# Kernel tuning notes

Measured on AMD Instinct MI355X. Metric: run time of the kernel, lower is better.

The kernel has to match this reference:

```python
import jax, jax.numpy as jnp
import numpy as np

B, T, D_IN, E, H = 2, 2048, 1024, 64, 16  # batch, num_tokens, input dim, emb_size(per-head), num_heads


def setup_inputs() -> dict:
    key = jax.random.key(0)
    ks = jax.random.split(key, 6)
    s = 0.02
    inp = jax.random.normal(ks[0], (B, T, D_IN), dtype=jnp.float32)
    # causal mask: 1.0 where attention is disallowed (j > i), matching `scaled_compat -= mask * 1e9`
    mask = jnp.triu(jnp.ones((T, T), dtype=jnp.float32), k=1)
    Wq = jax.random.normal(ks[1], (D_IN, E * H), dtype=jnp.float32) * s
    Wk = jax.random.normal(ks[2], (D_IN, E * H), dtype=jnp.float32) * s
    Wv = jax.random.normal(ks[3], (D_IN, E * H), dtype=jnp.float32) * s
    Wu = jax.random.normal(ks[4], (E * H, E), dtype=jnp.float32) * s
    bu = jnp.zeros((E,), dtype=jnp.float32)
    return {"inp": inp, "mask": mask, "Wq": Wq, "Wk": Wk, "Wv": Wv, "Wu": Wu, "bu": bu}


def reference(inp, mask, Wq, Wk, Wv, Wu, bu):
    b = inp.shape[0]
    q = inp @ Wq  # [B,T,E*H]
    k = inp @ Wk
    v = inp @ Wv
    # NOTE: original reshapes last dim as (E, H) -> heads on fastest axis (interleaved layout)
    q = q.reshape(b, T, E, H)
    k = k.reshape(b, T, E, H)
    v = v.reshape(b, T, E, H)
    scores = jnp.einsum("bteh,bseh->bhts", q, k) / jnp.sqrt(jnp.float32(E))  # [B,H,T,T]
    if mask is not None:
        scores = scores - mask * 1e9
    attn = jax.nn.softmax(scores, axis=-1)
    wv = jnp.einsum("bhts,bseh->bhte", attn, v)  # [B,H,T,E]
    # transpose [0,2,3,1] -> [B,T,E,H], then flatten to [B,T,E*H] (H fastest, matching original)
    wv = jnp.transpose(wv, (0, 2, 3, 1)).reshape(b, T, E * H)
    return wv @ Wu + bu  # unify Dense(emb_size), with bias
```

## Files before the change

kernel.cpp:

```cpp
#include <hip/hip_runtime.h>


typedef __bf16 bf16x8 __attribute__((ext_vector_type(8)));
typedef float f32x4 __attribute__((ext_vector_type(4)));
typedef unsigned short u16;
typedef unsigned int u32;

#define AS1 __attribute__((address_space(1)))
#define AS3 __attribute__((address_space(3)))

__device__ __forceinline__ void gll16(const void* g, void* l) {
    __builtin_amdgcn_global_load_lds((const AS1 u32*)g, (AS3 u32*)l, 16, 0, 0);
}

__device__ __forceinline__ u16 f2bf(float f) {
    union { float f; u32 u; } v; v.f = f;
    u32 r = (v.u + 0x7FFFu + ((v.u >> 16) & 1u)) >> 16;
    return (u16)r;
}

#define MM 4096
#define SCALE_LOG2E 0.18033688011112042f

__global__ void cast_x(const float* __restrict__ in, u16* __restrict__ out, int n4) {
    int i = blockIdx.x * blockDim.x + threadIdx.x;
    if (i < n4) {
        float4 f = ((const float4*)in)[i];
        ushort4 o;
        o.x = f2bf(f.x); o.y = f2bf(f.y); o.z = f2bf(f.z); o.w = f2bf(f.w);
        ((ushort4*)out)[i] = o;
    }
}

__global__ void transpose_w(const float* __restrict__ Wq, const float* __restrict__ Wk,
                            const float* __restrict__ Wv, const float* __restrict__ Wu,
                            u16* __restrict__ wqt, u16* __restrict__ wkt,
                            u16* __restrict__ wvt, u16* __restrict__ wut) {
    int z = blockIdx.z;
    const float* src; u16* dst; int N;
    if (z == 0)      { src = Wq; dst = wqt; N = 1024; }
    else if (z == 1) { src = Wk; dst = wkt; N = 1024; }
    else if (z == 2) { src = Wv; dst = wvt; N = 1024; }
    else             { src = Wu; dst = wut; N = 64; if (blockIdx.y >= 2) return; }
    __shared__ float lds[32][33];
    int k0 = blockIdx.x * 32, n0 = blockIdx.y * 32;
    int tid = threadIdx.x;
    int c = tid & 31, r0 = tid >> 5;
#pragma unroll
    for (int p = 0; p < 4; ++p) {
        int r = r0 + p * 8;
        lds[r][c] = src[(k0 + r) * N + n0 + c];
    }
    __syncthreads();
#pragma unroll
    for (int p = 0; p < 4; ++p) {
        int n = n0 + r0 + p * 8;
        if (z < 3) {
            int rnew = ((n & 15) << 6) | (n >> 4);
            dst[rnew * 1024 + k0 + c] = f2bf(lds[c][n - n0]);
        } else {
            int k = k0 + c;
            int kp = ((k & 15) << 6) | (k >> 4);
            dst[n * 1024 + kp] = f2bf(lds[c][n - n0]);
        }
    }
}

__global__ __launch_bounds__(256) void gemm_qkv(const u16* __restrict__ xb,
                                                const u16* __restrict__ wqt,
                                                const u16* __restrict__ wkt,
                                                const u16* __restrict__ wvt,
                                                u16* __restrict__ qh, u16* __restrict__ kh,
                                                u16* __restrict__ vh) {
    int z = blockIdx.z;
    const u16* wt = (z == 0) ? wqt : (z == 1) ? wkt : wvt;
    u16* dst      = (z == 0) ? qh  : (z == 1) ? kh  : vh;
    __shared__ u16 lA[3][128 * 32];
    __shared__ u16 lB[3][128 * 32];
    int tid = threadIdx.x;
    int m0 = blockIdx.x * 128, n0 = blockIdx.y * 128;
    int lane = tid & 63, w = tid >> 6;
    int wr = w >> 1, wc = w & 1;
    int l15 = lane & 15, quad = lane >> 4;
    f32x4 acc[4][4] = {};
    int srow = tid >> 2, scol = (tid & 3) * 8;
    const u16* ga = xb + (m0 + srow) * 1024 + scol;
    const u16* gb = wt + (n0 + srow) * 1024 + scol;
#pragma unroll
    for (int t0 = 0; t0 < 2; ++t0)
#pragma unroll
        for (int pp = 0; pp < 2; ++pp) {
            gll16(ga + pp * 65536 + t0 * 32, lA[t0] + (pp * 256 + tid) * 8);
            gll16(gb + pp * 65536 + t0 * 32, lB[t0] + (pp * 256 + tid) * 8);
        }
    int cur = 0;
#pragma unroll 1
    for (int kk = 0; kk < 32; ++kk) {
        if (kk < 31) asm volatile("s_waitcnt vmcnt(4)" ::: "memory");
        else         asm volatile("s_waitcnt vmcnt(0)" ::: "memory");
        __builtin_amdgcn_s_barrier();
        if (kk + 2 < 32) {
            int nxt = cur + 2; if (nxt >= 3) nxt -= 3;
            int kb = (kk + 2) * 32;
#pragma unroll
            for (int pp = 0; pp < 2; ++pp) {
                gll16(ga + pp * 65536 + kb, lA[nxt] + (pp * 256 + tid) * 8);
                gll16(gb + pp * 65536 + kb, lB[nxt] + (pp * 256 + tid) * 8);
            }
        }
        bf16x8 af[4], bfr[4];
#pragma unroll
        for (int i = 0; i < 4; ++i)
            af[i] = *(const bf16x8*)(lA[cur] + (wr * 64 + i * 16 + l15) * 32 + quad * 8);
#pragma unroll
        for (int j = 0; j < 4; ++j)
            bfr[j] = *(const bf16x8*)(lB[cur] + (wc * 64 + j * 16 + l15) * 32 + quad * 8);
#pragma unroll
        for (int i = 0; i < 4; ++i)
#pragma unroll
            for (int j = 0; j < 4; ++j)
                acc[i][j] = __builtin_amdgcn_mfma_f32_16x16x32_bf16(af[i], bfr[j], acc[i][j], 0, 0, 0);
        ++cur; if (cur == 3) cur = 0;
    }
    int bb = m0 >> 11;
    int hb = (n0 >> 6) + wc;
    if (z < 2) {
        float scale = (z == 0) ? SCALE_LOG2E : 1.f;
#pragma unroll
        for (int i = 0; i < 4; ++i)
#pragma unroll
            for (int r = 0; r < 4; ++r) {
                int m = m0 + wr * 64 + i * 16 + quad * 4 + r;
                ushort4 o;
                o.x = f2bf(acc[i][0][r] * scale); o.y = f2bf(acc[i][1][r] * scale);
                o.z = f2bf(acc[i][2][r] * scale); o.w = f2bf(acc[i][3][r] * scale);
                *(ushort4*)(dst + m * 1024 + hb * 64 + l15 * 4) = o;
            }
    } else {
#pragma unroll
        for (int j = 0; j < 4; ++j)
#pragma unroll
            for (int r = 0; r < 4; ++r) {
                ushort4 o;
                o.x = f2bf(acc[0][j][r]); o.y = f2bf(acc[1][j][r]);
                o.z = f2bf(acc[2][j][r]); o.w = f2bf(acc[3][j][r]);
                *(ushort4*)(dst + (((bb * 16 + hb) * 64) + j * 16 + l15) * 2048 +
                            (m0 & 2047) + wr * 64 + (quad * 4 + r) * 4) = o;
            }
    }
}

__global__ __launch_bounds__(256) void attn(const u16* __restrict__ qh, const u16* __restrict__ kh,
                                            const u16* __restrict__ vh, u16* __restrict__ ot,
                                            float* __restrict__ part, float* __restrict__ lp) {
    __shared__ u16 smem[25600];
    u16* sPQ = smem;
    const int tid = threadIdx.x;
    const int lane = tid & 63, w = tid >> 6;
    const int quad = lane >> 4, l15 = lane & 15;
    const int s = blockIdx.x, by = blockIdx.y;
    int qt, j0, j1, half;
    if (s < 8)       { qt = 7 - s;  j0 = 0;      j1 = 2 * qt + 2; half = -1; }
    else if (s < 16) { qt = s;      j0 = 0;      j1 = qt + 1;     half = 0;  }
    else             { qt = s - 8;  j0 = qt + 1; j1 = 2 * qt + 2; half = 1;  }
    const int b = by >> 4, h = by & 15;
    const int row0 = tid >> 3;
    const int cb0 = (tid & 7) ^ (row0 & 7);
    const u16* kg0 = kh + (b * 2048) * 1024 + h * 64 + row0 * 1024 + cb0 * 8;
    const u16* vg0 = vh + (by * 64) * 2048 + row0 * 2048 + cb0 * 8;
    const int fsw = (l15 & 7) * 8;

    const u16* qg = qh + (b * 2048 + qt * 128) * 1024 + h * 64;
#pragma unroll
    for (int p = 0; p < 4; ++p) {
        int c = p * 256 + tid;
        gll16(qg + (c >> 3) * 1024 + (c & 7) * 8, sPQ + c * 8);
    }
    __syncthreads();
    bf16x8 aq[2][2];
#pragma unroll
    for (int rg = 0; rg < 2; ++rg)
#pragma unroll
        for (int k2 = 0; k2 < 2; ++k2)
            aq[rg][k2] = *(const bf16x8*)(sPQ + (w * 32 + rg * 16 + l15) * 64 + k2 * 32 + quad * 8);

    {
        u16* sK0 = smem + 9216;
        u16* sV0 = smem + 17408;
        gll16(kg0 + j0 * 65536,         sK0 + tid * 8);
        gll16(kg0 + j0 * 65536 + 32768, sK0 + (256 + tid) * 8);
        gll16(vg0 + j0 * 64,            sV0 + tid * 8);
        gll16(vg0 + j0 * 64 + 65536,    sV0 + (256 + tid) * 8);
    }
    float lpart[2][4] = {};
    f32x4 oacc[2][4] = {};
    u16* sPw = sPQ + w * 2304;
    for (int jt = j0; jt < j1; ++jt) {
        int cur = (jt - j0) & 1;
        u16* sK = smem + 9216 + cur * 4096;
        u16* sV = smem + 17408 + cur * 4096;
        asm volatile("s_waitcnt vmcnt(0)" ::: "memory");
        __builtin_amdgcn_s_barrier();
        if (jt + 1 < j1) {
            u16* sKn = smem + 9216 + (cur ^ 1) * 4096;
            u16* sVn = smem + 17408 + (cur ^ 1) * 4096;
            gll16(kg0 + (jt + 1) * 65536,         sKn + tid * 8);
            gll16(kg0 + (jt + 1) * 65536 + 32768, sKn + (256 + tid) * 8);
            gll16(vg0 + (jt + 1) * 64,            sVn + tid * 8);
            gll16(vg0 + (jt + 1) * 64 + 65536,    sVn + (256 + tid) * 8);
        }
        f32x4 sacc[2][4] = {};
#pragma unroll
        for (int j4 = 0; j4 < 4; ++j4)
#pragma unroll
            for (int k2 = 0; k2 < 2; ++k2) {
                bf16x8 bk = *(const bf16x8*)(sK + (j4 * 16 + l15) * 64 + (((k2 * 4 + quad) * 8) ^ fsw));
                sacc[0][j4] = __builtin_amdgcn_mfma_f32_16x16x32_bf16(aq[0][k2], bk, sacc[0][j4], 0, 0, 0);
                sacc[1][j4] = __builtin_amdgcn_mfma_f32_16x16x32_bf16(aq[1][k2], bk, sacc[1][j4], 0, 0, 0);
            }
        if (jt >= 2 * qt) {
            int soff = (jt - 2 * qt) * 64;
#pragma unroll
            for (int rg = 0; rg < 2; ++rg)
#pragma unroll
                for (int j4 = 0; j4 < 4; ++j4)
#pragma unroll
                    for (int r = 0; r < 4; ++r) {
                        int sg = soff + j4 * 16 + l15;
                        int tg = w * 32 + rg * 16 + quad * 4 + r;
                        if (sg > tg) sacc[rg][j4][r] = -1e30f;
                    }
        }
#pragma unroll
        for (int rg = 0; rg < 2; ++rg)
#pragma unroll
            for (int j4 = 0; j4 < 4; ++j4)
#pragma unroll
                for (int r = 0; r < 4; ++r) {
                    float pe = __builtin_amdgcn_exp2f(sacc[rg][j4][r]);
                    sacc[rg][j4][r] = pe;
                    lpart[rg][r] += pe;
                }
#pragma unroll
        for (int rg = 0; rg < 2; ++rg)
#pragma unroll
            for (int r = 0; r < 4; ++r) {
                ushort4 o;
                o.x = f2bf(sacc[rg][0][r]); o.y = f2bf(sacc[rg][1][r]);
                o.z = f2bf(sacc[rg][2][r]); o.w = f2bf(sacc[rg][3][r]);
                *(ushort4*)(sPw + (rg * 16 + quad * 4 + r) * 72 + l15 * 4) = o;
            }
        bf16x8 ap[2][2];
#pragma unroll
        for (int rg = 0; rg < 2; ++rg)
#pragma unroll
            for (int k2 = 0; k2 < 2; ++k2)
                ap[rg][k2] = *(const bf16x8*)(sPw + (rg * 16 + l15) * 72 + k2 * 32 + quad * 8);
#pragma unroll
        for (int e4 = 0; e4 < 4; ++e4)
#pragma unroll
            for (int k2 = 0; k2 < 2; ++k2) {
                bf16x8 bv = *(const bf16x8*)(sV + (e4 * 16 + l15) * 64 + (((k2 * 4 + quad) * 8) ^ fsw));
                oacc[0][e4] = __builtin_amdgcn_mfma_f32_16x16x32_bf16(ap[0][k2], bv, oacc[0][e4], 0, 0, 0);
                oacc[1][e4] = __builtin_amdgcn_mfma_f32_16x16x32_bf16(ap[1][k2], bv, oacc[1][e4], 0, 0, 0);
            }
    }
    if (half < 0) {
#pragma unroll
        for (int rg = 0; rg < 2; ++rg)
#pragma unroll
            for (int r = 0; r < 4; ++r) {
                float rs = lpart[rg][r];
#pragma unroll
                for (int off = 1; off < 16; off <<= 1) rs += __shfl_xor(rs, off, 16);
                float inv = 1.f / rs;
                int t = qt * 128 + w * 32 + rg * 16 + quad * 4 + r;
                int base = (b * 2048 + t) * 1024 + h * 64;
#pragma unroll
                for (int e4 = 0; e4 < 4; ++e4)
                    ot[base + e4 * 16 + l15] = f2bf(oacc[rg][e4][r] * inv);
            }
    } else {
        int pb = by * 8 + (qt - 8);
        float* pg = part + (pb * 2 + half) * 8192;
        float* lg = lp + pb * 256 + half * 128;
#pragma unroll
        for (int rg = 0; rg < 2; ++rg)
#pragma unroll
            for (int r = 0; r < 4; ++r) {
                float rs = lpart[rg][r];
#pragma unroll
                for (int off = 1; off < 16; off <<= 1) rs += __shfl_xor(rs, off, 16);
                int row = w * 32 + rg * 16 + quad * 4 + r;
                if (l15 == 0) lg[row] = rs;
#pragma unroll
                for (int e4 = 0; e4 < 4; ++e4)
                    pg[row * 64 + e4 * 16 + l15] = oacc[rg][e4][r];
            }
    }
}

__global__ __launch_bounds__(256) void combine_o(const float* __restrict__ part,
                                                 const float* __restrict__ lp,
                                                 u16* __restrict__ ot) {
    int pb = blockIdx.x, tid = threadIdx.x;
    int by = pb >> 3, qt = 8 + (pb & 7);
    int b = by >> 4, h = by & 15;
    const float* pA = part + pb * 16384;
    const float* pB = pA + 8192;
    const float* lA = lp + pb * 256;
    const float* lB = lA + 128;
#pragma unroll
    for (int p = 0; p < 8; ++p) {
        int e = p * 1024 + tid * 4;
        int row = e >> 6, col = e & 63;
        float4 a = *(const float4*)(pA + e);
        float4 c = *(const float4*)(pB + e);
        float inv = 1.f / (lA[row] + lB[row]);
        int t = qt * 128 + row;
        ushort4 o;
        o.x = f2bf((a.x + c.x) * inv); o.y = f2bf((a.y + c.y) * inv);
        o.z = f2bf((a.z + c.z) * inv); o.w = f2bf((a.w + c.w) * inv);
        *(ushort4*)(ot + (b * 2048 + t) * 1024 + h * 64 + col) = o;
    }
}

__global__ __launch_bounds__(256) void gemm_out(const u16* __restrict__ ot, const u16* __restrict__ wut,
                                                const float* __restrict__ bu, float* __restrict__ out) {
    __shared__ float red[4][1088];
    int tid = threadIdx.x, lane = tid & 63, w = tid >> 6;
    int quad = lane >> 4, l15 = lane & 15;
    int m0 = blockIdx.x * 16;
    f32x4 acc[4] = {};
    const u16* aptr = ot + (m0 + l15) * 1024 + w * 256 + quad * 8;
    const u16* bptr = wut + l15 * 1024 + w * 256 + quad * 8;
#pragma unroll
    for (int kk = 0; kk < 8; ++kk) {
        bf16x8 af = *(const bf16x8*)(aptr + kk * 32);
#pragma unroll
        for (int j = 0; j < 4; ++j) {
            bf16x8 bfr = *(const bf16x8*)(bptr + j * 16 * 1024 + kk * 32);
            acc[j] = __builtin_amdgcn_mfma_f32_16x16x32_bf16(af, bfr, acc[j], 0, 0, 0);
        }
    }
#pragma unroll
    for (int j = 0; j < 4; ++j)
#pragma unroll
        for (int r = 0; r < 4; ++r)
            red[w][(j * 16 + l15) * 17 + quad * 4 + r] = acc[j][r];
    __syncthreads();
    int n = tid & 63, mq = tid >> 6;
    float bias = bu[n];
#pragma unroll
    for (int i = 0; i < 4; ++i) {
        int m = mq * 4 + i;
        float s = red[0][n * 17 + m] + red[1][n * 17 + m] + red[2][n * 17 + m] + red[3][n * 17 + m];
        out[(m0 + m) * 64 + n] = s + bias;
    }
}

#define OFF_XB   0u
#define OFF_WQT  8388608u
#define OFF_WKT  10485760u
#define OFF_WVT  12582912u
#define OFF_WUT  14680064u
#define OFF_QH   14811136u
#define OFF_KH   23199744u
#define OFF_VH   31588352u
#define OFF_OT   OFF_XB
#define OFF_PART 39976960u
#define OFF_LP   56754176u

extern "C" void kernel_launch(void* const* d_in, const int* in_sizes, int n_in,
                              void* d_out, int out_size, void* d_ws, size_t ws_size,
                              hipStream_t stream) {
    (void)in_sizes; (void)n_in; (void)out_size; (void)ws_size;
    const float* inp = (const float*)d_in[0];
    const float* Wq = (const float*)d_in[2];
    const float* Wk = (const float*)d_in[3];
    const float* Wv = (const float*)d_in[4];
    const float* Wu = (const float*)d_in[5];
    const float* bu = (const float*)d_in[6];
    float* out = (float*)d_out;
    char* ws = (char*)d_ws;
    u16* xb  = (u16*)(ws + OFF_XB);
    u16* wqt = (u16*)(ws + OFF_WQT);
    u16* wkt = (u16*)(ws + OFF_WKT);
    u16* wvt = (u16*)(ws + OFF_WVT);
    u16* wut = (u16*)(ws + OFF_WUT);
    u16* qh  = (u16*)(ws + OFF_QH);
    u16* kh  = (u16*)(ws + OFF_KH);
    u16* vh  = (u16*)(ws + OFF_VH);
    u16* ot  = (u16*)(ws + OFF_OT);
    float* part = (float*)(ws + OFF_PART);
    float* lpw  = (float*)(ws + OFF_LP);

    cast_x<<<4096, 256, 0, stream>>>(inp, xb, (MM * 1024) / 4);
    transpose_w<<<dim3(32, 32, 4), 256, 0, stream>>>(Wq, Wk, Wv, Wu, wqt, wkt, wvt, wut);
    gemm_qkv<<<dim3(32, 8, 3), 256, 0, stream>>>(xb, wqt, wkt, wvt, qh, kh, vh);
    attn<<<dim3(24, 32), 256, 0, stream>>>(qh, kh, vh, ot, part, lpw);
    combine_o<<<256, 256, 0, stream>>>(part, lpw, ot);
    gemm_out<<<256, 256, 0, stream>>>(ot, wut, bu, out);
}
```

Measured before the change: 168.9 us.

## Merge prep kernels, use native bf16 conversion, add MFMA priority hints

New measurement: 162.7 us. 3.7% less time.

```diff
diff --git a/kernel.cpp b/kernel.cpp
--- a/kernel.cpp
+++ b/kernel.cpp
@@ -2,6 +2,7 @@
 
 
 typedef __bf16 bf16x8 __attribute__((ext_vector_type(8)));
+typedef __bf16 bf16x4 __attribute__((ext_vector_type(4)));
 typedef float f32x4 __attribute__((ext_vector_type(4)));
 typedef unsigned short u16;
 typedef unsigned int u32;
@@ -14,37 +15,36 @@
 }
 
 __device__ __forceinline__ u16 f2bf(float f) {
-    union { float f; u32 u; } v; v.f = f;
-    u32 r = (v.u + 0x7FFFu + ((v.u >> 16) & 1u)) >> 16;
-    return (u16)r;
+    __bf16 h = (__bf16)f;
+    union { __bf16 h; u16 u; } v; v.h = h; return v.u;
 }
 
 #define MM 4096
 #define SCALE_LOG2E 0.18033688011112042f
 
-__global__ void cast_x(const float* __restrict__ in, u16* __restrict__ out, int n4) {
-    int i = blockIdx.x * blockDim.x + threadIdx.x;
-    if (i < n4) {
+__global__ void prep(const float* __restrict__ in, u16* __restrict__ out,
+                     const float* __restrict__ Wq, const float* __restrict__ Wk,
+                     const float* __restrict__ Wv, const float* __restrict__ Wu,
+                     u16* __restrict__ wqt, u16* __restrict__ wkt,
+                     u16* __restrict__ wvt, u16* __restrict__ wut) {
+    __shared__ float lds[32][33];
+    int bid = blockIdx.x, tid = threadIdx.x;
+    if (bid < 4096) {
+        int i = bid * 256 + tid;
         float4 f = ((const float4*)in)[i];
-        ushort4 o;
-        o.x = f2bf(f.x); o.y = f2bf(f.y); o.z = f2bf(f.z); o.w = f2bf(f.w);
-        ((ushort4*)out)[i] = o;
-    }
-}
-
-__global__ void transpose_w(const float* __restrict__ Wq, const float* __restrict__ Wk,
-                            const float* __restrict__ Wv, const float* __restrict__ Wu,
-                            u16* __restrict__ wqt, u16* __restrict__ wkt,
-                            u16* __restrict__ wvt, u16* __restrict__ wut) {
-    int z = blockIdx.z;
+        bf16x4 o;
+        o[0] = (__bf16)f.x; o[1] = (__bf16)f.y; o[2] = (__bf16)f.z; o[3] = (__bf16)f.w;
+        ((bf16x4*)out)[i] = o;
+        return;
+    }
+    int bid2 = bid - 4096;
+    int z = bid2 >> 10, y = (bid2 >> 5) & 31, x = bid2 & 31;
     const float* src; u16* dst; int N;
     if (z == 0)      { src = Wq; dst = wqt; N = 1024; }
     else if (z == 1) { src = Wk; dst = wkt; N = 1024; }
     else if (z == 2) { src = Wv; dst = wvt; N = 1024; }
-    else             { src = Wu; dst = wut; N = 64; if (blockIdx.y >= 2) return; }
-    __shared__ float lds[32][33];
-    int k0 = blockIdx.x * 32, n0 = blockIdx.y * 32;
-    int tid = threadIdx.x;
+    else             { src = Wu; dst = wut; N = 64; if (y >= 2) return; }
+    int k0 = x * 32, n0 = y * 32;
     int c = tid & 31, r0 = tid >> 5;
 #pragma unroll
     for (int p = 0; p < 4; ++p) {
@@ -131,21 +131,21 @@
 #pragma unroll
             for (int r = 0; r < 4; ++r) {
                 int m = m0 + wr * 64 + i * 16 + quad * 4 + r;
-                ushort4 o;
-                o.x = f2bf(acc[i][0][r] * scale); o.y = f2bf(acc[i][1][r] * scale);
-                o.z = f2bf(acc[i][2][r] * scale); o.w = f2bf(acc[i][3][r] * scale);
-                *(ushort4*)(dst + m * 1024 + hb * 64 + l15 * 4) = o;
+                bf16x4 o;
+                o[0] = (__bf16)(acc[i][0][r] * scale); o[1] = (__bf16)(acc[i][1][r] * scale);
+                o[2] = (__bf16)(acc[i][2][r] * scale); o[3] = (__bf16)(acc[i][3][r] * scale);
+                *(bf16x4*)(dst + m * 1024 + hb * 64 + l15 * 4) = o;
             }
     } else {
 #pragma unroll
         for (int j = 0; j < 4; ++j)
 #pragma unroll
             for (int r = 0; r < 4; ++r) {
-                ushort4 o;
-                o.x = f2bf(acc[0][j][r]); o.y = f2bf(acc[1][j][r]);
-                o.z = f2bf(acc[2][j][r]); o.w = f2bf(acc[3][j][r]);
-                *(ushort4*)(dst + (((bb * 16 + hb) * 64) + j * 16 + l15) * 2048 +
-                            (m0 & 2047) + wr * 64 + (quad * 4 + r) * 4) = o;
+                bf16x4 o;
+                o[0] = (__bf16)acc[0][j][r]; o[1] = (__bf16)acc[1][j][r];
+                o[2] = (__bf16)acc[2][j][r]; o[3] = (__bf16)acc[3][j][r];
+                *(bf16x4*)(dst + (((bb * 16 + hb) * 64) + j * 16 + l15) * 2048 +
+                           (m0 & 2047) + wr * 64 + (quad * 4 + r) * 4) = o;
             }
     }
 }
@@ -210,6 +210,7 @@
             gll16(vg0 + (jt + 1) * 64 + 65536,    sVn + (256 + tid) * 8);
         }
         f32x4 sacc[2][4] = {};
+        __builtin_amdgcn_s_setprio(1);
 #pragma unroll
         for (int j4 = 0; j4 < 4; ++j4)
 #pragma unroll
@@ -218,6 +219,7 @@
                 sacc[0][j4] = __builtin_amdgcn_mfma_f32_16x16x32_bf16(aq[0][k2], bk, sacc[0][j4], 0, 0, 0);
                 sacc[1][j4] = __builtin_amdgcn_mfma_f32_16x16x32_bf16(aq[1][k2], bk, sacc[1][j4], 0, 0, 0);
             }
+        __builtin_amdgcn_s_setprio(0);
         if (jt >= 2 * qt) {
             int soff = (jt - 2 * qt) * 64;
 #pragma unroll
@@ -234,21 +236,15 @@
 #pragma unroll
         for (int rg = 0; rg < 2; ++rg)
 #pragma unroll
-            for (int j4 = 0; j4 < 4; ++j4)
-#pragma unroll
-                for (int r = 0; r < 4; ++r) {
-                    float pe = __builtin_amdgcn_exp2f(sacc[rg][j4][r]);
-                    sacc[rg][j4][r] = pe;
-                    lpart[rg][r] += pe;
-                }
-#pragma unroll
-        for (int rg = 0; rg < 2; ++rg)
-#pragma unroll
             for (int r = 0; r < 4; ++r) {
-                ushort4 o;
-                o.x = f2bf(sacc[rg][0][r]); o.y = f2bf(sacc[rg][1][r]);
-                o.z = f2bf(sacc[rg][2][r]); o.w = f2bf(sacc[rg][3][r]);
-                *(ushort4*)(sPw + (rg * 16 + quad * 4 + r) * 72 + l15 * 4) = o;
+                float p0 = __builtin_amdgcn_exp2f(sacc[rg][0][r]);
+                float p1 = __builtin_amdgcn_exp2f(sacc[rg][1][r]);
+                float p2 = __builtin_amdgcn_exp2f(sacc[rg][2][r]);
+                float p3 = __builtin_amdgcn_exp2f(sacc[rg][3][r]);
+                lpart[rg][r] += (p0 + p1) + (p2 + p3);
+                bf16x4 o;
+                o[0] = (__bf16)p0; o[1] = (__bf16)p1; o[2] = (__bf16)p2; o[3] = (__bf16)p3;
+                *(bf16x4*)(sPw + (rg * 16 + quad * 4 + r) * 72 + l15 * 4) = o;
             }
         bf16x8 ap[2][2];
 #pragma unroll
@@ -256,6 +252,7 @@
 #pragma unroll
             for (int k2 = 0; k2 < 2; ++k2)
                 ap[rg][k2] = *(const bf16x8*)(sPw + (rg * 16 + l15) * 72 + k2 * 32 + quad * 8);
+        __builtin_amdgcn_s_setprio(1);
 #pragma unroll
         for (int e4 = 0; e4 < 4; ++e4)
 #pragma unroll
@@ -264,6 +261,7 @@
                 oacc[0][e4] = __builtin_amdgcn_mfma_f32_16x16x32_bf16(ap[0][k2], bv, oacc[0][e4], 0, 0, 0);
                 oacc[1][e4] = __builtin_amdgcn_mfma_f32_16x16x32_bf16(ap[1][k2], bv, oacc[1][e4], 0, 0, 0);
             }
+        __builtin_amdgcn_s_setprio(0);
     }
     if (half < 0) {
 #pragma unroll
@@ -318,10 +316,10 @@
         float4 c = *(const float4*)(pB + e);
         float inv = 1.f / (lA[row] + lB[row]);
         int t = qt * 128 + row;
-        ushort4 o;
-        o.x = f2bf((a.x + c.x) * inv); o.y = f2bf((a.y + c.y) * inv);
-        o.z = f2bf((a.z + c.z) * inv); o.w = f2bf((a.w + c.w) * inv);
-        *(ushort4*)(ot + (b * 2048 + t) * 1024 + h * 64 + col) = o;
+        bf16x4 o;
+        o[0] = (__bf16)((a.x + c.x) * inv); o[1] = (__bf16)((a.y + c.y) * inv);
+        o[2] = (__bf16)((a.z + c.z) * inv); o[3] = (__bf16)((a.w + c.w) * inv);
+        *(bf16x4*)(ot + (b * 2048 + t) * 1024 + h * 64 + col) = o;
     }
 }
 
@@ -395,8 +393,7 @@
     float* part = (float*)(ws + OFF_PART);
     float* lpw  = (float*)(ws + OFF_LP);
 
-    cast_x<<<4096, 256, 0, stream>>>(inp, xb, (MM * 1024) / 4);
-    transpose_w<<<dim3(32, 32, 4), 256, 0, stream>>>(Wq, Wk, Wv, Wu, wqt, wkt, wvt, wut);
+    prep<<<8192, 256, 0, stream>>>(inp, xb, Wq, Wk, Wv, Wu, wqt, wkt, wvt, wut);
     gemm_qkv<<<dim3(32, 8, 3), 256, 0, stream>>>(xb, wqt, wkt, wvt, qh, kh, vh);
     attn<<<dim3(24, 32), 256, 0, stream>>>(qh, kh, vh, ot, part, lpw);
     combine_o<<<256, 256, 0, stream>>>(part, lpw, ot);
```
